# Performance work log

Measured on AMD Instinct MI355X. Metric: run time of the kernel, lower is better.

Reference implementation:

```python
import jax, jax.numpy as jnp
import numpy as np

BS, NE, NQ, IN_DIM, EMBED_DIM, OUT_DIM, N_HEADS = 512, 256, 64, 512, 512, 512, 8
HEAD_DIM = EMBED_DIM // N_HEADS


def setup_inputs() -> dict:
    key = jax.random.key(0)
    k1, k2, k3, k4, k5, k6 = jax.random.split(key, 6)
    entities = jax.random.normal(k1, (BS, NE, IN_DIM), dtype=jnp.float32)
    pre_mask = jax.random.randint(k2, (BS, NQ, NE), 0, 2, dtype=jnp.int32)
    post_mask = jax.random.randint(k3, (BS, NQ), 0, 2, dtype=jnp.int32)
    W_in = jax.random.normal(k4, (IN_DIM, 3 * EMBED_DIM), dtype=jnp.float32) / np.sqrt(IN_DIM)
    W_out = jax.random.normal(k5, (EMBED_DIM, OUT_DIM), dtype=jnp.float32) / np.sqrt(EMBED_DIM)
    b_out = jax.random.normal(k6, (OUT_DIM,), dtype=jnp.float32) * 0.01
    return {"entities": entities, "pre_mask": pre_mask, "post_mask": post_mask,
            "W_in": W_in, "W_out": W_out, "b_out": b_out}


def reference(entities, pre_mask, post_mask, W_in, W_out, b_out):
    bs, ne, _ = entities.shape
    nq = post_mask.shape[1]
    scale = jnp.sqrt(jnp.asarray(HEAD_DIM, dtype=entities.dtype))
    # fused QKV projection (no bias), chunk order q, k, v
    qkv = entities @ W_in                                   # [bs, ne, 3*ed]
    q, k, v = jnp.split(qkv, 3, axis=-1)
    q = q[:, :nq]                                           # queries only for agents
    q = q.reshape(bs, nq, N_HEADS, HEAD_DIM)
    k = k.reshape(bs, ne, N_HEADS, HEAD_DIM)
    v = v.reshape(bs, ne, N_HEADS, HEAD_DIM)
    logits = jnp.einsum('bqhd,bkhd->bhqk', q, k) / scale    # [bs, h, nq, ne]
    mask = pre_mask[:, :nq].astype(bool)[:, None, :, :]     # [bs, 1, nq, ne]
    masked = jnp.where(mask, -jnp.inf, logits)
    w = jax.nn.softmax(masked, axis=-1)
    w = jnp.where(jnp.isnan(w), 0.0, w)                     # NaN-safe (all-masked rows)
    attn = jnp.einsum('bhqk,bkhd->bqhd', w, v).reshape(bs, nq, EMBED_DIM)
    out = attn @ W_out + b_out                              # [bs, nq, out_dim]
    out = jnp.where(post_mask.astype(bool)[:, :, None], 0.0, out)
    return out
```

## Files before the change

### kernel.cpp

```cpp
#include <hip/hip_runtime.h>
#include <hip/hip_bf16.h>

#define BS 512
#define NE 256
#define NQ 64
#define IN_DIM 512
#define EMBED_DIM 512
#define OUT_DIM 512
#define N_HEADS 8
#define HEAD_DIM 64

#define NEG_INF (-__builtin_inff())

typedef __attribute__((ext_vector_type(8))) short bf16x8;
typedef __attribute__((ext_vector_type(4))) float f32x4;
typedef __attribute__((ext_vector_type(4))) unsigned short u16x4;
typedef unsigned short ushort_t;

__device__ __forceinline__ unsigned short f2bf(float x) {
    unsigned u = __builtin_bit_cast(unsigned, x);
    unsigned r = (u + 0x7FFFu + ((u >> 16) & 1u)) >> 16;
    return (unsigned short)r;
}
__device__ __forceinline__ float bf2f(unsigned short h) {
    unsigned u = ((unsigned)h) << 16;
    return __builtin_bit_cast(float, u);
}

__global__ __launch_bounds__(256)
void transpose_split(const float* __restrict__ src, int R, int C,
                     ushort_t* __restrict__ dh, ushort_t* __restrict__ dl)
{
    int idx = blockIdx.x * 256 + threadIdx.x;
    if (idx >= R * C) return;
    int r = idx / C, c = idx % C;
    float x = src[idx];
    unsigned short h = f2bf(x);
    dh[(long long)c * R + r] = h;
    dl[(long long)c * R + r] = f2bf(x - bf2f(h));
}

template<int WR, int WC, bool ASPLIT, bool EPI>
__global__ __launch_bounds__(256)
void gemm_split(const float* __restrict__ Af,
                const ushort_t* __restrict__ Aph, const ushort_t* __restrict__ Apl,
                long long strideA, int lda,
                const ushort_t* __restrict__ Bth, const ushort_t* __restrict__ Btl,
                int ldbt,
                float* __restrict__ C, long long strideC, int ldc, int K,
                const float* __restrict__ bias, const int* __restrict__ post_mask)
{
    constexpr int BM = WR * 64;
    constexpr int BN = WC * 64;
    constexpr int PSA = BM * 8 + 4;
    constexpr int PSB = BN * 8 + 4;
    const int b = blockIdx.z;
    const int row0 = blockIdx.y * BM;
    const int col0 = blockIdx.x * BN;
    const int tid = threadIdx.x;
    const int l = tid & 63;
    const int w = tid >> 6;
    const int wr = w / WC;
    const int wc = w % WC;
    const int kg = l >> 4;
    const int lr = l & 15;

    __shared__ __align__(16) ushort_t sAh[4 * PSA];
    __shared__ __align__(16) ushort_t sAl[4 * PSA];
    __shared__ __align__(16) ushort_t sBh[4 * PSB];
    __shared__ __align__(16) ushort_t sBl[4 * PSB];

    f32x4 acc[4][4];
#pragma unroll
    for (int i = 0; i < 4; ++i)
#pragma unroll
        for (int j = 0; j < 4; ++j) acc[i][j] = f32x4{0.f, 0.f, 0.f, 0.f};

    for (int k0 = 0; k0 < K; k0 += 32) {
        __syncthreads();
        if constexpr (!ASPLIT) {
            const float* Ab = Af + (long long)b * strideA;
#pragma unroll
            for (int i = 0; i < BM * 8 / 256; ++i) {
                int idx = tid + i * 256;
                int row = idx >> 3, kq = idx & 7;
                float4 v = *(const float4*)(Ab + (long long)(row0 + row) * lda + k0 + kq * 4);
                u16x4 hv, lv;
                unsigned short h;
                h = f2bf(v.x); hv.x = h; lv.x = f2bf(v.x - bf2f(h));
                h = f2bf(v.y); hv.y = h; lv.y = f2bf(v.y - bf2f(h));
                h = f2bf(v.z); hv.z = h; lv.z = f2bf(v.z - bf2f(h));
                h = f2bf(v.w); hv.w = h; lv.w = f2bf(v.w - bf2f(h));
                int base = (kq >> 1) * PSA + row * 8 + (kq & 1) * 4;
                *(u16x4*)&sAh[base] = hv;
                *(u16x4*)&sAl[base] = lv;
            }
        } else {
            const ushort_t* Abh = Aph + (long long)b * strideA;
            const ushort_t* Abl = Apl + (long long)b * strideA;
#pragma unroll
            for (int i = 0; i < BM * 4 / 256; ++i) {
                int idx = tid + i * 256;
                int row = idx >> 2, g = idx & 3;
                *(float4*)&sAh[g * PSA + row * 8] =
                    *(const float4*)(Abh + (long long)(row0 + row) * lda + k0 + g * 8);
                *(float4*)&sAl[g * PSA + row * 8] =
                    *(const float4*)(Abl + (long long)(row0 + row) * lda + k0 + g * 8);
            }
        }
#pragma unroll
        for (int i = 0; i < BN * 4 / 256; ++i) {
            int idx = tid + i * 256;
            int c = idx >> 2, g = idx & 3;
            *(float4*)&sBh[g * PSB + c * 8] =
                *(const float4*)(Bth + (long long)(col0 + c) * ldbt + k0 + g * 8);
            *(float4*)&sBl[g * PSB + c * 8] =
                *(const float4*)(Btl + (long long)(col0 + c) * ldbt + k0 + g * 8);
        }
        __syncthreads();

        bf16x8 ah[4], al[4], bh[4], bl[4];
#pragma unroll
        for (int mi = 0; mi < 4; ++mi) {
            int r = wr * 64 + mi * 16 + lr;
            ah[mi] = *(const bf16x8*)&sAh[kg * PSA + r * 8];
            al[mi] = *(const bf16x8*)&sAl[kg * PSA + r * 8];
        }
#pragma unroll
        for (int ni = 0; ni < 4; ++ni) {
            int c = wc * 64 + ni * 16 + lr;
            bh[ni] = *(const bf16x8*)&sBh[kg * PSB + c * 8];
            bl[ni] = *(const bf16x8*)&sBl[kg * PSB + c * 8];
        }
#pragma unroll
        for (int mi = 0; mi < 4; ++mi)
#pragma unroll
            for (int ni = 0; ni < 4; ++ni) {
                f32x4 t = acc[mi][ni];
                t = __builtin_amdgcn_mfma_f32_16x16x32_bf16(ah[mi], bh[ni], t, 0, 0, 0);
                t = __builtin_amdgcn_mfma_f32_16x16x32_bf16(al[mi], bh[ni], t, 0, 0, 0);
                t = __builtin_amdgcn_mfma_f32_16x16x32_bf16(ah[mi], bl[ni], t, 0, 0, 0);
                acc[mi][ni] = t;
            }
    }

    float* Cb = C + (long long)b * strideC;
#pragma unroll
    for (int mi = 0; mi < 4; ++mi) {
        int rowb = row0 + wr * 64 + mi * 16 + kg * 4;
#pragma unroll
        for (int ni = 0; ni < 4; ++ni) {
            int col = col0 + wc * 64 + ni * 16 + lr;
#pragma unroll
            for (int j = 0; j < 4; ++j) {
                float x = acc[mi][ni][j];
                if constexpr (EPI) {
                    x += bias[col];
                    if (post_mask[b * NQ + rowb + j]) x = 0.f;
                }
                Cb[(long long)(rowb + j) * ldc + col] = x;
            }
        }
    }
}

__global__ __launch_bounds__(256)
void attn_f32(const float* __restrict__ Q,
              const float* __restrict__ KV,
              const int* __restrict__ pre_mask,
              ushort_t* __restrict__ ATTh, ushort_t* __restrict__ ATTl)
{
    const int h = blockIdx.x;
    const int b = blockIdx.y;
    const int tid = threadIdx.x;
    const int qg = tid >> 4;
    const int s  = tid & 15;

    __shared__ float Qs[64][68];
    __shared__ float Ts[64][68];

    {
        const float* src = Q + (long long)b * NQ * EMBED_DIM + h * HEAD_DIM;
#pragma unroll
        for (int i = 0; i < 4; ++i) {
            int f = tid + i * 256;
            int r = f >> 4, c4 = f & 15;
            *(float4*)&Qs[r][c4 * 4] = *(const float4*)(src + (long long)r * EMBED_DIM + c4 * 4);
        }
    }

    float wreg[4][16];
    const long long kvbase = (long long)b * NE * (2 * EMBED_DIM) + h * HEAD_DIM;
    const long long pmbase = ((long long)b * NQ) * NE;

#pragma unroll
    for (int et = 0; et < 4; ++et) {
        __syncthreads();
        {
            const float* src = KV + kvbase + (long long)(et * 64) * (2 * EMBED_DIM);
#pragma unroll
            for (int i = 0; i < 4; ++i) {
                int f = tid + i * 256;
                int r = f >> 4, c4 = f & 15;
                *(float4*)&Ts[r][c4 * 4] =
                    *(const float4*)(src + (long long)r * (2 * EMBED_DIM) + c4 * 4);
            }
        }
        int pm[4][4];
#pragma unroll
        for (int jj = 0; jj < 4; ++jj)
#pragma unroll
            for (int c = 0; c < 4; ++c)
                pm[jj][c] = pre_mask[pmbase + (long long)(qg + 16 * jj) * NE + et * 64 + c * 16 + s];
        __syncthreads();

        float lac[4][4];
#pragma unroll
        for (int jj = 0; jj < 4; ++jj)
#pragma unroll
            for (int c = 0; c < 4; ++c) lac[jj][c] = 0.f;

#pragma unroll 4
        for (int d4 = 0; d4 < 16; ++d4) {
            float4 rq0 = *(const float4*)&Qs[qg +  0][d4 * 4];
            float4 rq1 = *(const float4*)&Qs[qg + 16][d4 * 4];
            float4 rq2 = *(const float4*)&Qs[qg + 32][d4 * 4];
            float4 rq3 = *(const float4*)&Qs[qg + 48][d4 * 4];
#pragma unroll
            for (int c = 0; c < 4; ++c) {
                float4 rt = *(const float4*)&Ts[c * 16 + s][d4 * 4];
                lac[0][c] += rq0.x * rt.x + rq0.y * rt.y + rq0.z * rt.z + rq0.w * rt.w;
                lac[1][c] += rq1.x * rt.x + rq1.y * rt.y + rq1.z * rt.z + rq1.w * rt.w;
                lac[2][c] += rq2.x * rt.x + rq2.y * rt.y + rq2.z * rt.z + rq2.w * rt.w;
                lac[3][c] += rq3.x * rt.x + rq3.y * rt.y + rq3.z * rt.z + rq3.w * rt.w;
            }
        }
#pragma unroll
        for (int jj = 0; jj < 4; ++jj)
#pragma unroll
            for (int c = 0; c < 4; ++c)
                wreg[jj][et * 4 + c] = pm[jj][c] ? NEG_INF : lac[jj][c] * 0.125f;
    }

#pragma unroll
    for (int jj = 0; jj < 4; ++jj) {
        float m = NEG_INF;
#pragma unroll
        for (int r = 0; r < 16; ++r) m = fmaxf(m, wreg[jj][r]);
        m = fmaxf(m, __shfl_xor(m, 1));
        m = fmaxf(m, __shfl_xor(m, 2));
        m = fmaxf(m, __shfl_xor(m, 4));
        m = fmaxf(m, __shfl_xor(m, 8));
        float sum = 0.f;
#pragma unroll
        for (int r = 0; r < 16; ++r) {
            float p = (wreg[jj][r] == NEG_INF) ? 0.f : __expf(wreg[jj][r] - m);
            wreg[jj][r] = p;
            sum += p;
        }
        sum += __shfl_xor(sum, 1);
        sum += __shfl_xor(sum, 2);
        sum += __shfl_xor(sum, 4);
        sum += __shfl_xor(sum, 8);
        float inv = (sum > 0.f) ? (1.0f / sum) : 0.f;
#pragma unroll
        for (int r = 0; r < 16; ++r) wreg[jj][r] *= inv;
    }

    float oacc[4][4];
#pragma unroll
    for (int jj = 0; jj < 4; ++jj)
#pragma unroll
        for (int k = 0; k < 4; ++k) oacc[jj][k] = 0.f;

#pragma unroll
    for (int et = 0; et < 4; ++et) {
        __syncthreads();
        {
            const float* src = KV + kvbase + (long long)(et * 64) * (2 * EMBED_DIM) + EMBED_DIM;
#pragma unroll
            for (int i = 0; i < 4; ++i) {
                int f = tid + i * 256;
                int r = f >> 4, c4 = f & 15;
                *(float4*)&Ts[r][c4 * 4] =
                    *(const float4*)(src + (long long)r * (2 * EMBED_DIM) + c4 * 4);
            }
        }
#pragma unroll
        for (int jj = 0; jj < 4; ++jj)
#pragma unroll
            for (int c = 0; c < 4; ++c)
                Qs[qg + 16 * jj][c * 16 + s] = wreg[jj][et * 4 + c];
        __syncthreads();

#pragma unroll 4
        for (int el = 0; el < 64; ++el) {
            float4 rv = *(const float4*)&Ts[el][s * 4];
            float p0 = Qs[qg +  0][el];
            float p1 = Qs[qg + 16][el];
            float p2 = Qs[qg + 32][el];
            float p3 = Qs[qg + 48][el];
            oacc[0][0] += p0 * rv.x; oacc[0][1] += p0 * rv.y; oacc[0][2] += p0 * rv.z; oacc[0][3] += p0 * rv.w;
            oacc[1][0] += p1 * rv.x; oacc[1][1] += p1 * rv.y; oacc[1][2] += p1 * rv.z; oacc[1][3] += p1 * rv.w;
            oacc[2][0] += p2 * rv.x; oacc[2][1] += p2 * rv.y; oacc[2][2] += p2 * rv.z; oacc[2][3] += p2 * rv.w;
            oacc[3][0] += p3 * rv.x; oacc[3][1] += p3 * rv.y; oacc[3][2] += p3 * rv.z; oacc[3][3] += p3 * rv.w;
        }
    }

#pragma unroll
    for (int jj = 0; jj < 4; ++jj) {
        long long off = ((long long)b * NQ + qg + 16 * jj) * EMBED_DIM + h * HEAD_DIM + s * 4;
        u16x4 hv, lv;
#pragma unroll
        for (int k = 0; k < 4; ++k) {
            float x = oacc[jj][k];
            unsigned short hh = f2bf(x);
            ((unsigned short*)&hv)[k] = hh;
            ((unsigned short*)&lv)[k] = f2bf(x - bf2f(hh));
        }
        *(u16x4*)(ATTh + off) = hv;
        *(u16x4*)(ATTl + off) = lv;
    }
}

extern "C" void kernel_launch(void* const* d_in, const int* in_sizes, int n_in,
                              void* d_out, int out_size, void* d_ws, size_t ws_size,
                              hipStream_t stream)
{
    const float* entities  = (const float*)d_in[0];
    const int*   pre_mask  = (const int*)d_in[1];
    const int*   post_mask = (const int*)d_in[2];
    const float* W_in      = (const float*)d_in[3];
    const float* W_out     = (const float*)d_in[4];
    const float* b_out     = (const float*)d_in[5];
    float* out = (float*)d_out;

    float* Qb  = (float*)d_ws;
    float* KVb = Qb + (size_t)BS * NQ * EMBED_DIM;
    ushort_t* ATTh = (ushort_t*)(KVb + (size_t)BS * NE * 2 * EMBED_DIM);
    ushort_t* ATTl = ATTh + (size_t)BS * NQ * EMBED_DIM;
    ushort_t* Wth  = ATTl + (size_t)BS * NQ * EMBED_DIM;
    ushort_t* Wtl  = Wth + (size_t)(3 * EMBED_DIM) * IN_DIM;
    ushort_t* Woth = Wtl + (size_t)(3 * EMBED_DIM) * IN_DIM;
    ushort_t* Wotl = Woth + (size_t)OUT_DIM * EMBED_DIM;

    transpose_split<<<(IN_DIM * 3 * EMBED_DIM + 255) / 256, 256, 0, stream>>>(
        W_in, IN_DIM, 3 * EMBED_DIM, Wth, Wtl);
    transpose_split<<<(EMBED_DIM * OUT_DIM + 255) / 256, 256, 0, stream>>>(
        W_out, EMBED_DIM, OUT_DIM, Woth, Wotl);

    gemm_split<1, 4, false, false><<<dim3(EMBED_DIM / 256, 1, BS), 256, 0, stream>>>(
        entities, nullptr, nullptr, (long long)NE * IN_DIM, IN_DIM,
        Wth, Wtl, IN_DIM,
        Qb, (long long)NQ * EMBED_DIM, EMBED_DIM, IN_DIM,
        nullptr, nullptr);

    gemm_split<2, 2, false, false><<<dim3(2 * EMBED_DIM / 128, NE / 128, BS), 256, 0, stream>>>(
        entities, nullptr, nullptr, (long long)NE * IN_DIM, IN_DIM,
        Wth + (size_t)EMBED_DIM * IN_DIM, Wtl + (size_t)EMBED_DIM * IN_DIM, IN_DIM,
        KVb, (long long)NE * 2 * EMBED_DIM, 2 * EMBED_DIM, IN_DIM,
        nullptr, nullptr);

    attn_f32<<<dim3(N_HEADS, BS), 256, 0, stream>>>(Qb, KVb, pre_mask, ATTh, ATTl);

    gemm_split<1, 4, true, true><<<dim3(OUT_DIM / 256, 1, BS), 256, 0, stream>>>(
        nullptr, ATTh, ATTl, (long long)NQ * EMBED_DIM, EMBED_DIM,
        Woth, Wotl, EMBED_DIM,
        out, (long long)NQ * OUT_DIM, OUT_DIM, EMBED_DIM,
        b_out, post_mask);
}
```

Before: 1.412 ms.

## Pre-split entities into MFMA-tiled bf16 layout and load GEMM tiles via global_load_lds

```diff
diff --git a/kernel.cpp b/kernel.cpp
--- a/kernel.cpp
+++ b/kernel.cpp
@@ -15,6 +15,7 @@
 typedef __attribute__((ext_vector_type(8))) short bf16x8;
 typedef __attribute__((ext_vector_type(4))) float f32x4;
 typedef __attribute__((ext_vector_type(4))) unsigned short u16x4;
+typedef __attribute__((ext_vector_type(8))) unsigned short u16x8;
 typedef unsigned short ushort_t;
 
 __device__ __forceinline__ unsigned short f2bf(float x) {
@@ -27,33 +28,78 @@
     return __builtin_bit_cast(float, u);
 }
 
+__device__ __forceinline__ void gload16(const ushort_t* gsrc, ushort_t* ldst) {
+    __builtin_amdgcn_global_load_lds(
+        (const __attribute__((address_space(1))) unsigned int*)gsrc,
+        (__attribute__((address_space(3))) unsigned int*)ldst, 16, 0, 0);
+}
+
 __global__ __launch_bounds__(256)
-void transpose_split(const float* __restrict__ src, int R, int C,
-                     ushort_t* __restrict__ dh, ushort_t* __restrict__ dl)
+void esplit(const float* __restrict__ E, ushort_t* __restrict__ Eh, ushort_t* __restrict__ El)
 {
-    int idx = blockIdx.x * 256 + threadIdx.x;
-    if (idx >= R * C) return;
-    int r = idx / C, c = idx % C;
-    float x = src[idx];
-    unsigned short h = f2bf(x);
-    dh[(long long)c * R + r] = h;
-    dl[(long long)c * R + r] = f2bf(x - bf2f(h));
-}
-
-template<int WR, int WC, bool ASPLIT, bool EPI>
+    const int b  = blockIdx.x >> 4;
+    const int kb = blockIdx.x & 15;
+    const int tid = threadIdx.x;
+    constexpr int PS = 256 * 8 + 8;
+    __shared__ __align__(16) ushort_t sh[4 * PS];
+    __shared__ __align__(16) ushort_t sl[4 * PS];
+
+    const float* src = E + (long long)b * NE * IN_DIM + kb * 32;
+#pragma unroll
+    for (int i = 0; i < 8; ++i) {
+        int f = tid + i * 256;
+        int row = f >> 3, kq = f & 7;
+        float4 v = *(const float4*)(src + (long long)row * IN_DIM + kq * 4);
+        u16x4 hv, lv;
+        unsigned short h;
+        h = f2bf(v.x); hv.x = h; lv.x = f2bf(v.x - bf2f(h));
+        h = f2bf(v.y); hv.y = h; lv.y = f2bf(v.y - bf2f(h));
+        h = f2bf(v.z); hv.z = h; lv.z = f2bf(v.z - bf2f(h));
+        h = f2bf(v.w); hv.w = h; lv.w = f2bf(v.w - bf2f(h));
+        int base = (kq >> 1) * PS + row * 8 + (kq & 1) * 4;
+        *(u16x4*)&sh[base] = hv;
+        *(u16x4*)&sl[base] = lv;
+    }
+    __syncthreads();
+    const long long G0 = ((long long)b * 16 + kb) * 1024;
+#pragma unroll
+    for (int i = 0; i < 4; ++i) {
+        int c = tid + i * 256;
+        int la = (c >> 8) * PS + (c & 255) * 8;
+        *(float4*)(Eh + (G0 + c) * 8) = *(const float4*)&sh[la];
+        *(float4*)(El + (G0 + c) * 8) = *(const float4*)&sl[la];
+    }
+}
+
 __global__ __launch_bounds__(256)
-void gemm_split(const float* __restrict__ Af,
-                const ushort_t* __restrict__ Aph, const ushort_t* __restrict__ Apl,
-                long long strideA, int lda,
-                const ushort_t* __restrict__ Bth, const ushort_t* __restrict__ Btl,
-                int ldbt,
-                float* __restrict__ C, long long strideC, int ldc, int K,
-                const float* __restrict__ bias, const int* __restrict__ post_mask)
+void wsplit(const float* __restrict__ src, int C, int nchunks,
+            ushort_t* __restrict__ dh, ushort_t* __restrict__ dl)
+{
+    int c = blockIdx.x * 256 + threadIdx.x;
+    if (c >= nchunks) return;
+    int kchunk = c / C, col = c - kchunk * C;
+    const float* s = src + (long long)(kchunk * 8) * C + col;
+    u16x8 hv, lv;
+#pragma unroll
+    for (int j = 0; j < 8; ++j) {
+        float x = s[(long long)j * C];
+        unsigned short h = f2bf(x);
+        hv[j] = h; lv[j] = f2bf(x - bf2f(h));
+    }
+    *(u16x8*)(dh + (long long)c * 8) = hv;
+    *(u16x8*)(dl + (long long)c * 8) = lv;
+}
+
+template<int WR, int WC, int RA, bool EPI>
+__global__ __launch_bounds__(256)
+void gemm_glds(const ushort_t* __restrict__ Ah, const ushort_t* __restrict__ Al,
+               const ushort_t* __restrict__ Bh, const ushort_t* __restrict__ Bl,
+               int RB, int colOfs,
+               float* __restrict__ C, long long strideC, int ldc,
+               const float* __restrict__ bias, const int* __restrict__ post_mask)
 {
     constexpr int BM = WR * 64;
     constexpr int BN = WC * 64;
-    constexpr int PSA = BM * 8 + 4;
-    constexpr int PSB = BN * 8 + 4;
     const int b = blockIdx.z;
     const int row0 = blockIdx.y * BM;
     const int col0 = blockIdx.x * BN;
@@ -65,10 +111,24 @@
     const int kg = l >> 4;
     const int lr = l & 15;
 
-    __shared__ __align__(16) ushort_t sAh[4 * PSA];
-    __shared__ __align__(16) ushort_t sAl[4 * PSA];
-    __shared__ __align__(16) ushort_t sBh[4 * PSB];
-    __shared__ __align__(16) ushort_t sBl[4 * PSB];
+    __shared__ __align__(16) ushort_t sAh[4 * BM * 8], sAl[4 * BM * 8];
+    __shared__ __align__(16) ushort_t sBh[4 * BN * 8], sBl[4 * BN * 8];
+
+    const ushort_t* pAh[WR]; const ushort_t* pAl[WR];
+    const ushort_t* pBh[WC]; const ushort_t* pBl[WC];
+    const long long abase = (long long)b * 64 * RA * 8;
+#pragma unroll
+    for (int j = 0; j < WR; ++j) {
+        long long g = ((long long)w * RA + row0 + j * 64 + l) * 8;
+        pAh[j] = Ah + abase + g;
+        pAl[j] = Al + abase + g;
+    }
+#pragma unroll
+    for (int j = 0; j < WC; ++j) {
+        long long g = ((long long)w * RB + colOfs + col0 + j * 64 + l) * 8;
+        pBh[j] = Bh + g;
+        pBl[j] = Bl + g;
+    }
 
     f32x4 acc[4][4];
 #pragma unroll
@@ -76,61 +136,36 @@
 #pragma unroll
         for (int j = 0; j < 4; ++j) acc[i][j] = f32x4{0.f, 0.f, 0.f, 0.f};
 
-    for (int k0 = 0; k0 < K; k0 += 32) {
-        __syncthreads();
-        if constexpr (!ASPLIT) {
-            const float* Ab = Af + (long long)b * strideA;
-#pragma unroll
-            for (int i = 0; i < BM * 8 / 256; ++i) {
-                int idx = tid + i * 256;
-                int row = idx >> 3, kq = idx & 7;
-                float4 v = *(const float4*)(Ab + (long long)(row0 + row) * lda + k0 + kq * 4);
-                u16x4 hv, lv;
-                unsigned short h;
-                h = f2bf(v.x); hv.x = h; lv.x = f2bf(v.x - bf2f(h));
-                h = f2bf(v.y); hv.y = h; lv.y = f2bf(v.y - bf2f(h));
-                h = f2bf(v.z); hv.z = h; lv.z = f2bf(v.z - bf2f(h));
-                h = f2bf(v.w); hv.w = h; lv.w = f2bf(v.w - bf2f(h));
-                int base = (kq >> 1) * PSA + row * 8 + (kq & 1) * 4;
-                *(u16x4*)&sAh[base] = hv;
-                *(u16x4*)&sAl[base] = lv;
-            }
-        } else {
-            const ushort_t* Abh = Aph + (long long)b * strideA;
-            const ushort_t* Abl = Apl + (long long)b * strideA;
-#pragma unroll
-            for (int i = 0; i < BM * 4 / 256; ++i) {
-                int idx = tid + i * 256;
-                int row = idx >> 2, g = idx & 3;
-                *(float4*)&sAh[g * PSA + row * 8] =
-                    *(const float4*)(Abh + (long long)(row0 + row) * lda + k0 + g * 8);
-                *(float4*)&sAl[g * PSA + row * 8] =
-                    *(const float4*)(Abl + (long long)(row0 + row) * lda + k0 + g * 8);
-            }
-        }
-#pragma unroll
-        for (int i = 0; i < BN * 4 / 256; ++i) {
-            int idx = tid + i * 256;
-            int c = idx >> 2, g = idx & 3;
-            *(float4*)&sBh[g * PSB + c * 8] =
-                *(const float4*)(Bth + (long long)(col0 + c) * ldbt + k0 + g * 8);
-            *(float4*)&sBl[g * PSB + c * 8] =
-                *(const float4*)(Btl + (long long)(col0 + c) * ldbt + k0 + g * 8);
-        }
+    for (int kb = 0; kb < 16; ++kb) {
+#pragma unroll
+        for (int j = 0; j < WR; ++j) {
+            gload16(pAh[j], &sAh[(w * BM + j * 64) * 8]);
+            gload16(pAl[j], &sAl[(w * BM + j * 64) * 8]);
+            pAh[j] += 4LL * RA * 8;
+            pAl[j] += 4LL * RA * 8;
+        }
+#pragma unroll
+        for (int j = 0; j < WC; ++j) {
+            gload16(pBh[j], &sBh[(w * BN + j * 64) * 8]);
+            gload16(pBl[j], &sBl[(w * BN + j * 64) * 8]);
+            pBh[j] += 4LL * RB * 8;
+            pBl[j] += 4LL * RB * 8;
+        }
+        asm volatile("s_waitcnt vmcnt(0)" ::: "memory");
         __syncthreads();
 
         bf16x8 ah[4], al[4], bh[4], bl[4];
 #pragma unroll
         for (int mi = 0; mi < 4; ++mi) {
             int r = wr * 64 + mi * 16 + lr;
-            ah[mi] = *(const bf16x8*)&sAh[kg * PSA + r * 8];
-            al[mi] = *(const bf16x8*)&sAl[kg * PSA + r * 8];
+            ah[mi] = *(const bf16x8*)&sAh[(kg * BM + r) * 8];
+            al[mi] = *(const bf16x8*)&sAl[(kg * BM + r) * 8];
         }
 #pragma unroll
         for (int ni = 0; ni < 4; ++ni) {
             int c = wc * 64 + ni * 16 + lr;
-            bh[ni] = *(const bf16x8*)&sBh[kg * PSB + c * 8];
-            bl[ni] = *(const bf16x8*)&sBl[kg * PSB + c * 8];
+            bh[ni] = *(const bf16x8*)&sBh[(kg * BN + c) * 8];
+            bl[ni] = *(const bf16x8*)&sBl[(kg * BN + c) * 8];
         }
 #pragma unroll
         for (int mi = 0; mi < 4; ++mi)
@@ -142,6 +177,7 @@
                 t = __builtin_amdgcn_mfma_f32_16x16x32_bf16(ah[mi], bl[ni], t, 0, 0, 0);
                 acc[mi][ni] = t;
             }
+        __syncthreads();
     }
 
     float* Cb = C + (long long)b * strideC;
@@ -307,9 +343,12 @@
         }
     }
 
+    const int kc = (h * 64 + s * 4) >> 3;
+    const int kb_ = kc >> 2, kg_ = kc & 3, half = s & 1;
 #pragma unroll
     for (int jj = 0; jj < 4; ++jj) {
-        long long off = ((long long)b * NQ + qg + 16 * jj) * EMBED_DIM + h * HEAD_DIM + s * 4;
+        int row = qg + 16 * jj;
+        long long g = ((((long long)b * 16 + kb_) * 4 + kg_) * 64 + row) * 8 + half * 4;
         u16x4 hv, lv;
 #pragma unroll
         for (int k = 0; k < 4; ++k) {
@@ -318,8 +357,8 @@
             ((unsigned short*)&hv)[k] = hh;
             ((unsigned short*)&lv)[k] = f2bf(x - bf2f(hh));
         }
-        *(u16x4*)(ATTh + off) = hv;
-        *(u16x4*)(ATTl + off) = lv;
+        *(u16x4*)(ATTh + g) = hv;
+        *(u16x4*)(ATTl + g) = lv;
     }
 }
 
@@ -337,35 +376,30 @@
 
     float* Qb  = (float*)d_ws;
     float* KVb = Qb + (size_t)BS * NQ * EMBED_DIM;
-    ushort_t* ATTh = (ushort_t*)(KVb + (size_t)BS * NE * 2 * EMBED_DIM);
-    ushort_t* ATTl = ATTh + (size_t)BS * NQ * EMBED_DIM;
-    ushort_t* Wth  = ATTl + (size_t)BS * NQ * EMBED_DIM;
-    ushort_t* Wtl  = Wth + (size_t)(3 * EMBED_DIM) * IN_DIM;
-    ushort_t* Woth = Wtl + (size_t)(3 * EMBED_DIM) * IN_DIM;
-    ushort_t* Wotl = Woth + (size_t)OUT_DIM * EMBED_DIM;
-
-    transpose_split<<<(IN_DIM * 3 * EMBED_DIM + 255) / 256, 256, 0, stream>>>(
-        W_in, IN_DIM, 3 * EMBED_DIM, Wth, Wtl);
-    transpose_split<<<(EMBED_DIM * OUT_DIM + 255) / 256, 256, 0, stream>>>(
-        W_out, EMBED_DIM, OUT_DIM, Woth, Wotl);
-
-    gemm_split<1, 4, false, false><<<dim3(EMBED_DIM / 256, 1, BS), 256, 0, stream>>>(
-        entities, nullptr, nullptr, (long long)NE * IN_DIM, IN_DIM,
-        Wth, Wtl, IN_DIM,
-        Qb, (long long)NQ * EMBED_DIM, EMBED_DIM, IN_DIM,
-        nullptr, nullptr);
-
-    gemm_split<2, 2, false, false><<<dim3(2 * EMBED_DIM / 128, NE / 128, BS), 256, 0, stream>>>(
-        entities, nullptr, nullptr, (long long)NE * IN_DIM, IN_DIM,
-        Wth + (size_t)EMBED_DIM * IN_DIM, Wtl + (size_t)EMBED_DIM * IN_DIM, IN_DIM,
-        KVb, (long long)NE * 2 * EMBED_DIM, 2 * EMBED_DIM, IN_DIM,
-        nullptr, nullptr);
+    ushort_t* Esph = (ushort_t*)(KVb + (size_t)BS * NE * 2 * EMBED_DIM);
+    ushort_t* Espl = Esph + (size_t)BS * 16 * 4 * 256 * 8;
+    ushort_t* Wsph = Espl + (size_t)BS * 16 * 4 * 256 * 8;
+    ushort_t* Wspl  = Wsph + (size_t)64 * 1536 * 8;
+    ushort_t* Wosph = Wspl + (size_t)64 * 1536 * 8;
+    ushort_t* Wospl = Wosph + (size_t)64 * 512 * 8;
+    ushort_t* ATTh = Esph;
+    ushort_t* ATTl = Espl;
+
+    wsplit<<<(64 * 1536 + 255) / 256, 256, 0, stream>>>(W_in, 3 * EMBED_DIM, 64 * 1536, Wsph, Wspl);
+    wsplit<<<(64 * 512 + 255) / 256, 256, 0, stream>>>(W_out, OUT_DIM, 64 * 512, Wosph, Wospl);
+    esplit<<<BS * 16, 256, 0, stream>>>(entities, Esph, Espl);
+
+    gemm_glds<1, 4, 256, false><<<dim3(2, 1, BS), 256, 0, stream>>>(
+        Esph, Espl, Wsph, Wspl, 3 * EMBED_DIM, 0,
+        Qb, (long long)NQ * EMBED_DIM, EMBED_DIM, nullptr, nullptr);
+
+    gemm_glds<2, 2, 256, false><<<dim3(8, 2, BS), 256, 0, stream>>>(
+        Esph, Espl, Wsph, Wspl, 3 * EMBED_DIM, EMBED_DIM,
+        KVb, (long long)NE * 2 * EMBED_DIM, 2 * EMBED_DIM, nullptr, nullptr);
 
     attn_f32<<<dim3(N_HEADS, BS), 256, 0, stream>>>(Qb, KVb, pre_mask, ATTh, ATTl);
 
-    gemm_split<1, 4, true, true><<<dim3(OUT_DIM / 256, 1, BS), 256, 0, stream>>>(
-        nullptr, ATTh, ATTl, (long long)NQ * EMBED_DIM, EMBED_DIM,
-        Woth, Wotl, EMBED_DIM,
-        out, (long long)NQ * OUT_DIM, OUT_DIM, EMBED_DIM,
-        b_out, post_mask);
-}
+    gemm_glds<1, 4, 64, true><<<dim3(2, 1, BS), 256, 0, stream>>>(
+        ATTh, ATTl, Wosph, Wospl, OUT_DIM, 0,
+        out, (long long)NQ * OUT_DIM, OUT_DIM, b_out, post_mask);
+}
```

Result: faster. 1.274 ms (-9.8%).
